# Optimization experiments

Measured on AMD Instinct MI355X. Metric: run time of the kernel, lower is better.

Reference implementation:

```python
import jax, jax.numpy as jnp
import numpy as np

D = 256; DFF = 1024; H = 8; L = 4; P = 4; NK = 18; NQ = 100; BS = 8; DH = D // H
SHAPES = ((100, 100), (50, 50), (25, 25), (13, 13))   # (H_l, W_l) per level
START = (0, 10000, 12500, 13125); LIN = 13294
PARAM_SHAPES = [
    ("across_in_w", (3 * D, D)), ("across_in_b", (3 * D,)), ("across_out_w", (D, D)), ("across_out_b", (D,)),
    ("within_in_w", (3 * D, D)), ("within_in_b", (3 * D,)), ("within_out_w", (D, D)), ("within_out_b", (D,)),
    ("off_w", (H * L * P * 2, D)), ("off_b", (H * L * P * 2,)), ("aw_w", (H * L * P, D)), ("aw_b", (H * L * P,)),
    ("val_w", (D, D)), ("val_b", (D,)), ("msout_w", (D, D)), ("msout_b", (D,)),
    ("lin1_w", (DFF, D)), ("lin1_b", (DFF,)), ("lin2_w", (D, DFF)), ("lin2_b", (D,)),
    ("lin1p_w", (DFF, D)), ("lin1p_b", (DFF,)), ("lin2p_w", (D, DFF)), ("lin2p_b", (D,)),
]
NORMS = ["across_norm", "within_norm", "norm1", "norm2", "norm2p"]
PNAMES = [n for n, _ in PARAM_SHAPES] + [n + s for n in NORMS for s in ("_g", "_b")]


def setup_inputs():
    ks = iter(jax.random.split(jax.random.key(0), 80))
    rn = lambda s, sc=1.0: jax.random.normal(next(ks), s, jnp.float32) * sc
    inp = {}
    inp["tgt_pose"] = rn((NQ, BS, NK, D))
    inp["tgt_pose_query_pos"] = rn((NQ, BS, NK, D))
    inp["tgt_pose_reference_points"] = jax.random.uniform(next(ks), (NQ * NK, BS, L, 2), jnp.float32)
    inp["memory"] = rn((LIN, BS, D))
    for n, s in PARAM_SHAPES:
        inp[n] = rn(s, 0.02)
    for n in NORMS:
        inp[n + "_g"] = 1.0 + rn((D,), 0.02)
        inp[n + "_b"] = rn((D,), 0.02)
    return inp


def _ln(x, g, b):
    mu = x.mean(-1, keepdims=True)
    xc = x - mu
    return xc * jax.lax.rsqrt((xc * xc).mean(-1, keepdims=True) + 1e-5) * g + b


def _mha(q, k, v, in_w, in_b, out_w, out_b, mask=None):
    # q,k,v: [S,B,D] (torch nn.MultiheadAttention layout)
    S, B, _ = q.shape
    def proj(x, i):
        return (x @ in_w[i * D:(i + 1) * D].T + in_b[i * D:(i + 1) * D]).reshape(-1, B, H, DH).transpose(1, 2, 0, 3)
    qh = proj(q, 0) * (DH ** -0.5); kh = proj(k, 1); vh = proj(v, 2)   # [B,H,S,DH]
    sc = jnp.einsum('bhqd,bhkd->bhqk', qh, kh)
    if mask is not None:
        sc = sc + mask
    o = jnp.einsum('bhqk,bhkd->bhqd', jax.nn.softmax(sc, -1), vh)
    return o.transpose(2, 0, 1, 3).reshape(S, B, D) @ out_w.T + out_b


def _msdeform(query, ref, mem, off_w, off_b, aw_w, aw_b, val_w, val_b, out_w, out_b):
    # query [N,Lq,D], ref [N,Lq,L,2] in [0,1] (x,y), mem [N,LIN,D]
    N, Lq, _ = query.shape
    value = (mem @ val_w.T + val_b).reshape(N, LIN, H, DH).transpose(0, 2, 1, 3)   # [N,H,LIN,DH]
    off = (query @ off_w.T + off_b).reshape(N, Lq, H, L, P, 2)
    aw = jax.nn.softmax((query @ aw_w.T + aw_b).reshape(N, Lq, H, L * P), -1).reshape(N, Lq, H, L, P)
    normalizer = jnp.array([[w, h] for (h, w) in SHAPES], jnp.float32)   # (W_l, H_l)
    loc = ref[:, :, None, :, None, :] + off / normalizer[None, None, None, :, None, :]   # [N,Lq,H,L,P,2]
    lvl_outs = []
    for li, (Hl, Wl) in enumerate(SHAPES):
        v_l = value[:, :, START[li]:START[li] + Hl * Wl]   # [N,H,Hl*Wl,DH]
        g = loc[:, :, :, li]                               # [N,Lq,H,P,2]
        # grid_sample(align_corners=False, padding_mode='zeros') on sampling grid 2*loc-1
        x = g[..., 0] * Wl - 0.5; y = g[..., 1] * Hl - 0.5
        x0 = jnp.floor(x); y0 = jnp.floor(y)
        lx = x - x0; ly = y - y0
        x0i = x0.astype(jnp.int32); y0i = y0.astype(jnp.int32)
        def gather(xi, yi):
            valid = ((xi >= 0) & (xi < Wl) & (yi >= 0) & (yi < Hl)).astype(v_l.dtype)
            idx = jnp.clip(yi, 0, Hl - 1) * Wl + jnp.clip(xi, 0, Wl - 1)   # [N,Lq,H,P]
            it = idx.transpose(0, 2, 1, 3).reshape(N, H, Lq * P)
            vt = jnp.take_along_axis(v_l, it[..., None], axis=2).reshape(N, H, Lq, P, DH)
            return vt * valid.transpose(0, 2, 1, 3)[..., None]
        wx = lx.transpose(0, 2, 1, 3)[..., None]; wy = ly.transpose(0, 2, 1, 3)[..., None]
        samp = (gather(x0i, y0i) * (1 - wx) * (1 - wy) + gather(x0i + 1, y0i) * wx * (1 - wy)
                + gather(x0i, y0i + 1) * (1 - wx) * wy + gather(x0i + 1, y0i + 1) * wx * wy)
        lvl_outs.append(samp)   # [N,H,Lq,P,DH]
    samp = jnp.stack(lvl_outs, 0)   # [L,N,H,Lq,P,DH]
    out = jnp.einsum('lnhqpd,nqhlp->nqhd', samp, aw).reshape(N, Lq, D)
    return out @ out_w.T + out_b


def _forward(tgt, pos, ref, mem, p):
    # 1) across-person self-attention along nq
    qf = tgt.reshape(NQ, BS * NK, D)
    t2 = _mha(qf, qf, qf, p['across_in_w'], p['across_in_b'], p['across_out_w'], p['across_out_b']).reshape(NQ, BS, NK, D)
    tgt = _ln(tgt + t2, p['across_norm_g'], p['across_norm_b'])
    # 2) deformable cross-attention; with_pos_embed mutates tgt in place in the original
    tgt = tgt + pos
    q = tgt.transpose(1, 0, 2, 3).reshape(BS, NQ * NK, D)
    t2 = _msdeform(q, ref.transpose(1, 0, 2, 3), mem.transpose(1, 0, 2),
                   p['off_w'], p['off_b'], p['aw_w'], p['aw_b'], p['val_w'], p['val_b'], p['msout_w'], p['msout_b'])
    t2 = t2.reshape(BS, NQ, NK, D).transpose(1, 0, 2, 3)
    tgt = _ln(tgt + t2, p['norm1_g'], p['norm1_b'])
    # 3) FFN
    t2 = jax.nn.relu(tgt @ p['lin1_w'].T + p['lin1_b']) @ p['lin2_w'].T + p['lin2_b']
    tgt = _ln(tgt + t2, p['norm2_g'], p['norm2_b'])
    # 4) within-pose self-attention (second in-place with_pos_embed)
    tgt = tgt + pos
    qw = tgt.reshape(NQ * BS, NK, D).transpose(1, 0, 2)
    mask = jnp.full((NK, NK), 1e-8, tgt.dtype)   # zero adjacency matrix additive mask
    t2 = _mha(qw, qw, qw, p['within_in_w'], p['within_in_b'], p['within_out_w'], p['within_out_b'], mask)
    t2 = t2.transpose(1, 0, 2).reshape(NQ, BS, NK, D)
    tgt = _ln(tgt + t2, p['within_norm_g'], p['within_norm_b'])
    # 5) late FFN
    t2 = jax.nn.relu(tgt @ p['lin1p_w'].T + p['lin1p_b']) @ p['lin2p_w'].T + p['lin2p_b']
    return _ln(tgt + t2, p['norm2p_g'], p['norm2p_b'])


def reference(tgt_pose, tgt_pose_query_pos, tgt_pose_reference_points, memory, across_in_w, across_in_b, across_out_w, across_out_b, within_in_w, within_in_b, within_out_w, within_out_b, off_w, off_b, aw_w, aw_b, val_w, val_b, msout_w, msout_b, lin1_w, lin1_b, lin2_w, lin2_b, lin1p_w, lin1p_b, lin2p_w, lin2p_b, across_norm_g, across_norm_b, within_norm_g, within_norm_b, norm1_g, norm1_b, norm2_g, norm2_b, norm2p_g, norm2p_b):
    _l = dict(locals())
    p = {n: _l[n] for n in PNAMES}
    return _forward(tgt_pose, tgt_pose_query_pos, tgt_pose_reference_points, memory, p)
```

## Files before the change

kernel.cpp:

```cpp
#include <hip/hip_runtime.h>
#include <cstdint>
#include <cstddef>

constexpr int D_   = 256;
constexpr int NK_  = 18;
constexpr int NQ_  = 100;
constexpr int BS_  = 8;
constexpr int T_   = NQ_ * BS_ * NK_;
constexpr int LIN_ = 13294;
constexpr int LQ_  = NQ_ * NK_;

typedef __attribute__((ext_vector_type(8))) short bfv8;
typedef __attribute__((ext_vector_type(4))) float f32x4;

__device__ __forceinline__ ushort f2b(float f) {
  uint32_t u = __builtin_bit_cast(uint32_t, f);
  u += 0x7fffu + ((u >> 16) & 1u);
  return (ushort)(u >> 16);
}
__device__ __forceinline__ float b2f(ushort h) {
  uint32_t u = ((uint32_t)h) << 16;
  return __builtin_bit_cast(float, u);
}
__device__ __forceinline__ uint pk2(float lo, float hi) {
  return (uint)f2b(lo) | ((uint)f2b(hi) << 16);
}
__device__ __forceinline__ void gload16(const ushort* g, ushort* l) {
  __builtin_amdgcn_global_load_lds(
      (const __attribute__((address_space(1))) void*)g,
      (__attribute__((address_space(3))) void*)l, 16, 0, 0);
}

constexpr int WOF0  = 0;
constexpr int WOF1  = 196608;
constexpr int WOF2  = 393216;
constexpr int WOF3  = 458752;
constexpr int WOF4  = 524288;
constexpr int WOF5  = 589824;
constexpr int WOF6  = 622592;
constexpr int WOF7  = 688128;
constexpr int WOF8  = 753664;
constexpr int WOF9  = 1015808;
constexpr int WOF10 = 1277952;
constexpr int WOF11 = 1540096;
constexpr int WTOT  = 1802240;

__global__ __launch_bounds__(256) void conv_weights(
    const float* __restrict__ w0, const float* __restrict__ w1,
    const float* __restrict__ w2, const float* __restrict__ w3,
    const float* __restrict__ w4, const float* __restrict__ w5,
    const float* __restrict__ w6, const float* __restrict__ w7,
    const float* __restrict__ w8, const float* __restrict__ w9,
    const float* __restrict__ w10, const float* __restrict__ w11,
    ushort* __restrict__ out) {
  int i8 = (blockIdx.x * 256 + threadIdx.x) * 8;
  if (i8 >= WTOT) return;
  const float* src; int off;
  if      (i8 < WOF1)  { src = w0;  off = WOF0; }
  else if (i8 < WOF2)  { src = w1;  off = WOF1; }
  else if (i8 < WOF3)  { src = w2;  off = WOF2; }
  else if (i8 < WOF4)  { src = w3;  off = WOF3; }
  else if (i8 < WOF5)  { src = w4;  off = WOF4; }
  else if (i8 < WOF6)  { src = w5;  off = WOF5; }
  else if (i8 < WOF7)  { src = w6;  off = WOF6; }
  else if (i8 < WOF8)  { src = w7;  off = WOF7; }
  else if (i8 < WOF9)  { src = w8;  off = WOF8; }
  else if (i8 < WOF10) { src = w9;  off = WOF9; }
  else if (i8 < WOF11) { src = w10; off = WOF10; }
  else                 { src = w11; off = WOF11; }
  const float4 v0 = *(const float4*)(src + (i8 - off));
  const float4 v1 = *(const float4*)(src + (i8 - off) + 4);
  uint4 o;
  o.x = pk2(v0.x, v0.y); o.y = pk2(v0.z, v0.w);
  o.z = pk2(v1.x, v1.y); o.w = pk2(v1.z, v1.w);
  *(uint4*)(out + i8) = o;
}

__global__ __launch_bounds__(384) void pack_bias(
    const float* __restrict__ off_b, const float* __restrict__ aw_b,
    float* __restrict__ out) {
  int t = threadIdx.x;
  out[t] = (t < 256) ? off_b[t] : aw_b[t - 256];
}

template<bool REORD>
__global__ __launch_bounds__(256) void conv_a_bf16(
    const float* __restrict__ in, ushort* __restrict__ out, int rows) {
  int idx = blockIdx.x * 256 + threadIdx.x;
  int r = idx >> 5, c = (idx & 31) * 8;
  if (r >= rows) return;
  int ro = r;
  if (REORD) { int i = r >> 3, b = r & 7; ro = b * LIN_ + i; }
  const float* p = in + (size_t)r * 256 + c;
  float4 v0 = *(const float4*)p, v1 = *(const float4*)(p + 4);
  uint4 o;
  o.x = pk2(v0.x, v0.y); o.y = pk2(v0.z, v0.w);
  o.z = pk2(v1.x, v1.y); o.w = pk2(v1.z, v1.w);
  *(uint4*)(out + (size_t)ro * 256 + c) = o;
}

template<int AMODE, int OUTMODE, int BM>
__global__ __launch_bounds__(256) void gemm_mfma(
    const ushort* __restrict__ A, const ushort* __restrict__ W,
    const float* __restrict__ bias, void* __restrict__ Cv,
    int M, int N, int K) {
  constexpr int AJ = BM / 64;
  constexpr int MR = BM / 32;
  __shared__ ushort As[BM * 32];
  __shared__ ushort Bs[128 * 32];
  const int tid = threadIdx.x;
  const int bm = blockIdx.y * BM, bn = blockIdx.x * 128;
  const int wave = tid >> 6, lane = tid & 63;

  const int srow = wave * 16 + (lane >> 2);
  const ushort* gA[AJ]; ushort* lA[AJ];
  const ushort* gB[2];  ushort* lB[2];
#pragma unroll
  for (int j = 0; j < AJ; ++j) {
    int row = j * 64 + srow;
    int gch = (lane & 3) ^ (row & 3);
    int gm = bm + row; if (gm >= M) gm = M - 1;
    int asrc;
    if (AMODE == 0) {
      asrc = gm;
    } else {
      int b = gm / LQ_, lq = gm - b * LQ_;
      int qq = lq / NK_, kk = lq - qq * NK_;
      asrc = qq * (BS_ * NK_) + b * NK_ + kk;
    }
    gA[j] = A + (size_t)asrc * K + gch * 8;
    lA[j] = As + (j * 4 + wave) * 512;
  }
#pragma unroll
  for (int j = 0; j < 2; ++j) {
    int row = j * 64 + srow;
    int gch = (lane & 3) ^ (row & 3);
    gB[j] = W + (size_t)(bn + row) * K + gch * 8;
    lB[j] = Bs + (j * 4 + wave) * 512;
  }

  const int wm = (wave >> 1) * (BM / 2), wn = (wave & 1) * 64;
  const int fr = lane & 15, fk = lane >> 4;
  const int sw = (fk ^ (fr & 3)) << 3;

  f32x4 acc[MR][4] = {};
  for (int k0 = 0; k0 < K; k0 += 32) {
#pragma unroll
    for (int j = 0; j < AJ; ++j) gload16(gA[j] + k0, lA[j]);
#pragma unroll
    for (int j = 0; j < 2; ++j) gload16(gB[j] + k0, lB[j]);
    __syncthreads();
    bfv8 a[MR], b[4];
#pragma unroll
    for (int m = 0; m < MR; ++m)
      a[m] = *(const bfv8*)&As[(wm + m * 16 + fr) * 32 + sw];
#pragma unroll
    for (int n = 0; n < 4; ++n)
      b[n] = *(const bfv8*)&Bs[(wn + n * 16 + fr) * 32 + sw];
#pragma unroll
    for (int m = 0; m < MR; ++m)
#pragma unroll
      for (int n = 0; n < 4; ++n)
        acc[m][n] = __builtin_amdgcn_mfma_f32_16x16x32_bf16(a[m], b[n], acc[m][n], 0, 0, 0);
    __syncthreads();
  }

  const int row0 = (lane >> 4) * 4;
  const int col = lane & 15;
#pragma unroll
  for (int m = 0; m < MR; ++m) {
#pragma unroll
    for (int n = 0; n < 4; ++n) {
      int cn = bn + wn + n * 16 + col;
      float bv = bias[cn];
#pragma unroll
      for (int j = 0; j < 4; ++j) {
        int mg = bm + wm + m * 16 + row0 + j;
        if (mg < M) {
          float o = acc[m][n][j] + bv;
          if (OUTMODE == 2) o = fmaxf(o, 0.f);
          if (OUTMODE == 0) ((float*)Cv)[(size_t)mg * N + cn] = o;
          else ((ushort*)Cv)[(size_t)mg * N + cn] = f2b(o);
        }
      }
    }
  }
}

template<int LNMODE>
__global__ __launch_bounds__(256) void gemm_ln(
    const ushort* __restrict__ A, const ushort* __restrict__ W,
    const float* __restrict__ bias, const float* __restrict__ X,
    const float* __restrict__ POS, const float* __restrict__ G,
    const float* __restrict__ Bb, float* __restrict__ CT,
    ushort* __restrict__ CTb, int K) {
  __shared__ float Ep[32][264];
  ushort* As = (ushort*)&Ep[0][0];
  ushort* Bs = As + 32 * 32;

  const int tid = threadIdx.x;
  const int wave = tid >> 6, lane = tid & 63;
  const int bm = blockIdx.x * 32;

  const int arow = wave * 8 + (lane >> 2);
  const int agch = (lane & 3) ^ (arow & 3);
  const ushort* gA = A + (size_t)(bm + arow) * K + agch * 8;
  ushort* lA = As + wave * 256;
  const int srow = wave * 16 + (lane >> 2);
  const ushort* gB[4]; ushort* lB[4];
#pragma unroll
  for (int j = 0; j < 4; ++j) {
    int row = j * 64 + srow;
    int gch = (lane & 3) ^ (row & 3);
    gB[j] = W + (size_t)row * K + gch * 8;
    lB[j] = Bs + (j * 4 + wave) * 512;
  }

  const int wn = wave * 64;
  const int fr = lane & 15, fk = lane >> 4;
  const int sw = (fk ^ (fr & 3)) << 3;

  f32x4 acc[2][4] = {};
  for (int k0 = 0; k0 < K; k0 += 32) {
    if (lane < 32) gload16(gA + k0, lA);
#pragma unroll
    for (int j = 0; j < 4; ++j) gload16(gB[j] + k0, lB[j]);
    __syncthreads();
    bfv8 a[2], b[4];
#pragma unroll
    for (int m = 0; m < 2; ++m)
      a[m] = *(const bfv8*)&As[(m * 16 + fr) * 32 + sw];
#pragma unroll
    for (int n = 0; n < 4; ++n)
      b[n] = *(const bfv8*)&Bs[(wn + n * 16 + fr) * 32 + sw];
#pragma unroll
    for (int m = 0; m < 2; ++m)
#pragma unroll
      for (int n = 0; n < 4; ++n)
        acc[m][n] = __builtin_amdgcn_mfma_f32_16x16x32_bf16(a[m], b[n], acc[m][n], 0, 0, 0);
    __syncthreads();
  }

  const int row0 = (lane >> 4) * 4;
  const int col = lane & 15;
  float bv[4];
#pragma unroll
  for (int n = 0; n < 4; ++n) bv[n] = bias[wn + n * 16 + col];

  const float4 g4 = *(const float4*)(G + lane * 4);
  const float4 bb4 = *(const float4*)(Bb + lane * 4);

#pragma unroll
  for (int m = 0; m < 2; ++m)
#pragma unroll
    for (int n = 0; n < 4; ++n)
#pragma unroll
      for (int j = 0; j < 4; ++j)
        Ep[m * 16 + row0 + j][wn + n * 16 + col] = acc[m][n][j] + bv[n];
  __syncthreads();

  for (int rr = 0; rr < 8; ++rr) {
    int lrow = wave * 8 + rr;
    size_t off = (size_t)(bm + lrow) * 256 + lane * 4;
    float4 ev = *(const float4*)&Ep[lrow][lane * 4];
    float4 xv = *(const float4*)(X + off);
    float4 v = make_float4(xv.x + ev.x, xv.y + ev.y, xv.z + ev.z, xv.w + ev.w);
    float s = v.x + v.y + v.z + v.w;
#pragma unroll
    for (int o = 32; o; o >>= 1) s += __shfl_xor(s, o);
    float mu = s * (1.0f / 256.0f);
    float4 c = make_float4(v.x - mu, v.y - mu, v.z - mu, v.w - mu);
    float q = c.x * c.x + c.y * c.y + c.z * c.z + c.w * c.w;
#pragma unroll
    for (int o = 32; o; o >>= 1) q += __shfl_xor(q, o);
    float rs = rsqrtf(q * (1.0f / 256.0f) + 1e-5f);
    float4 o4;
    o4.x = c.x * rs * g4.x + bb4.x;
    o4.y = c.y * rs * g4.y + bb4.y;
    o4.z = c.z * rs * g4.z + bb4.z;
    o4.w = c.w * rs * g4.w + bb4.w;
    if (LNMODE == 0) {
      float4 pv = *(const float4*)(POS + off);
      o4.x += pv.x; o4.y += pv.y; o4.z += pv.z; o4.w += pv.w;
    }
    *(float4*)(CT + off) = o4;
    if (LNMODE != 2) {
      ushort4 ob;
      ob.x = f2b(o4.x); ob.y = f2b(o4.y); ob.z = f2b(o4.z); ob.w = f2b(o4.w);
      *(ushort4*)(CTb + off) = ob;
    }
  }
}

__global__ __launch_bounds__(256) void attn_across_mfma(
    const ushort* __restrict__ QKV, ushort* __restrict__ O) {
  __shared__ ushort Qs[112][40];
  __shared__ ushort Ks[112][40];
  __shared__ ushort Vt[32][136];
  __shared__ ushort Ps[112][136];
  const int b = blockIdx.x >> 3, h = blockIdx.x & 7;
  const int tid = threadIdx.x;

  for (int idx = tid; idx < 112 * 16; idx += 256) {
    int r = idx >> 4, du = (idx & 15) * 2;
    uint q = 0, k = 0;
    if (r < 100) {
      size_t base = ((size_t)r * 144 + b) * 768 + h * 32 + du;
      q = *(const uint*)(QKV + base);
      k = *(const uint*)(QKV + base + 256);
    }
    *(uint*)&Qs[r][du] = q;
    *(uint*)&Ks[r][du] = k;
  }
  for (int idx = tid; idx < 128 * 32; idx += 256) {
    int s = idx >> 5, d = idx & 31;
    ushort v = 0;
    if (s < 100) v = QKV[((size_t)s * 144 + b) * 768 + 512 + h * 32 + d];
    Vt[d][s] = v;
  }
  for (int idx = tid; idx < 112 * 8; idx += 256) {
    int r = idx >> 3, c = 112 + (idx & 7) * 2;
    *(uint*)&Ps[r][c] = 0;
  }
  __syncthreads();

  const int wave = tid >> 6, lane = tid & 63;
  const int fr = lane & 15, fk = lane >> 4;
  const float scale = 0.17677669529663687f;

#pragma unroll
  for (int mi = 0; mi < 2; ++mi) {
    const int mt = wave + mi * 4;
    if (mt < 7) {
      bfv8 aq = *(const bfv8*)&Qs[mt * 16 + fr][fk * 8];
      f32x4 sacc[7];
#pragma unroll
      for (int nt = 0; nt < 7; ++nt) {
        bfv8 bk = *(const bfv8*)&Ks[nt * 16 + fr][fk * 8];
        f32x4 z = {0.f, 0.f, 0.f, 0.f};
        sacc[nt] = __builtin_amdgcn_mfma_f32_16x16x32_bf16(aq, bk, z, 0, 0, 0);
      }
      const bool maskc = (lane & 15) >= 4;
#pragma unroll
      for (int j = 0; j < 4; ++j) {
        float v[7];
        float mx = -1e30f;
#pragma unroll
        for (int nt = 0; nt < 7; ++nt) {
          float s = sacc[nt][j] * scale;
          if (nt == 6 && maskc) s = -1e30f;
          v[nt] = s;
          mx = fmaxf(mx, s);
        }
        mx = fmaxf(mx, __shfl_xor(mx, 1));
        mx = fmaxf(mx, __shfl_xor(mx, 2));
        mx = fmaxf(mx, __shfl_xor(mx, 4));
        mx = fmaxf(mx, __shfl_xor(mx, 8));
        float sum = 0.f;
#pragma unroll
        for (int nt = 0; nt < 7; ++nt) {
          v[nt] = __expf(v[nt] - mx);
          sum += v[nt];
        }
        sum += __shfl_xor(sum, 1);
        sum += __shfl_xor(sum, 2);
        sum += __shfl_xor(sum, 4);
        sum += __shfl_xor(sum, 8);
        float inv = 1.f / sum;
        int row = mt * 16 + (lane >> 4) * 4 + j;
#pragma unroll
        for (int nt = 0; nt < 7; ++nt)
          Ps[row][nt * 16 + (lane & 15)] = f2b(v[nt] * inv);
      }
    }
  }
  __syncthreads();

  f32x4 oacc[2][2] = {};
#pragma unroll
  for (int mi = 0; mi < 2; ++mi) {
    const int mt = wave + mi * 4;
    if (mt < 7) {
#pragma unroll
      for (int ks = 0; ks < 4; ++ks) {
        bfv8 ap = *(const bfv8*)&Ps[mt * 16 + fr][ks * 32 + fk * 8];
#pragma unroll
        for (int n = 0; n < 2; ++n) {
          bfv8 bv = *(const bfv8*)&Vt[n * 16 + fr][ks * 32 + fk * 8];
          oacc[mi][n] = __builtin_amdgcn_mfma_f32_16x16x32_bf16(ap, bv, oacc[mi][n], 0, 0, 0);
        }
      }
#pragma unroll
      for (int n = 0; n < 2; ++n) {
#pragma unroll
        for (int j = 0; j < 4; ++j) {
          int q = mt * 16 + (lane >> 4) * 4 + j;
          if (q < 100) {
            O[((size_t)q * 144 + b) * 256 + h * 32 + n * 16 + (lane & 15)] =
                f2b(oacc[mi][n][j]);
          }
        }
      }
    }
  }
}

__global__ __launch_bounds__(256) void attn_within(
    const ushort* __restrict__ QKV, ushort* __restrict__ O) {
  constexpr int ST = 258;
  __shared__ ushort Qs[18 * ST];
  __shared__ ushort Ks[18 * ST];
  __shared__ ushort Vs[18 * ST];
  const int bidx = blockIdx.x;
  const int qq = bidx >> 3, bb = bidx & 7;
  const int tid = threadIdx.x;
  for (int idx = tid; idx < 18 * 128; idx += 256) {
    int r = idx >> 7, j2 = (idx & 127) * 2;
    size_t base = ((size_t)qq * 144 + bb * 18 + r) * 768 + j2;
    *(uint*)&Qs[r * ST + j2] = *(const uint*)(QKV + base);
    *(uint*)&Ks[r * ST + j2] = *(const uint*)(QKV + base + 256);
    *(uint*)&Vs[r * ST + j2] = *(const uint*)(QKV + base + 512);
  }
  __syncthreads();
  const int wave = tid >> 6, lane = tid & 63;
  const int h = wave * 2 + (lane >> 5);
  const int li = lane & 31;
  const int hd = h * 32;
  const float scale = 0.17677669529663687f;
  const bool kv = li < 18;
  for (int s = 0; s < 18; ++s) {
    float sc = 0.f;
    if (kv) {
      const ushort* qrow = &Qs[s * ST + hd];
      const ushort* krow = &Ks[li * ST + hd];
#pragma unroll 8
      for (int d = 0; d < 32; ++d) sc += b2f(qrow[d]) * b2f(krow[d]);
    }
    sc = kv ? sc * scale : -1e30f;
    float mx = sc;
    mx = fmaxf(mx, __shfl_xor(mx, 16));
    mx = fmaxf(mx, __shfl_xor(mx, 8));
    mx = fmaxf(mx, __shfl_xor(mx, 4));
    mx = fmaxf(mx, __shfl_xor(mx, 2));
    mx = fmaxf(mx, __shfl_xor(mx, 1));
    float e = kv ? __expf(sc - mx) : 0.f;
    float sum = e;
    sum += __shfl_xor(sum, 16);
    sum += __shfl_xor(sum, 8);
    sum += __shfl_xor(sum, 4);
    sum += __shfl_xor(sum, 2);
    sum += __shfl_xor(sum, 1);
    float p = e / sum;
    float o = 0.f;
    const int half = lane & 32;
#pragma unroll
    for (int k = 0; k < 18; ++k) {
      float pk = __shfl(p, half + k);
      o += pk * b2f(Vs[k * ST + hd + li]);
    }
    O[((size_t)qq * 144 + bb * 18 + s) * 256 + hd + li] = f2b(o);
  }
}

__global__ __launch_bounds__(256) void deform_sample(
    const float* __restrict__ OFFAW, const ushort* __restrict__ V,
    const float* __restrict__ REF, ushort* __restrict__ OUT) {
  __shared__ uint2 sDesc[32 * 65];
  const int tid = threadIdx.x;
  const int m0 = blockIdx.x * 4;

  const int WH[4] = {100, 50, 25, 13};
  const int STl[4] = {0, 10000, 12500, 13125};

#pragma unroll
  for (int dd = 0; dd < 2; ++dd) {
    const int desc = tid + dd * 256;
    const int g = desc >> 7, rem = desc & 127;
    const int h = rem >> 4, lp = rem & 15, li = lp >> 2, p = lp & 3;
    const int m = m0 + g;
    const int b = m / LQ_, lq = m - b * LQ_;

    float awv = OFFAW[(size_t)m * 384 + 256 + h * 16 + lp];
    float mx = awv;
    mx = fmaxf(mx, __shfl_xor(mx, 8, 16));
    mx = fmaxf(mx, __shfl_xor(mx, 4, 16));
    mx = fmaxf(mx, __shfl_xor(mx, 2, 16));
    mx = fmaxf(mx, __shfl_xor(mx, 1, 16));
    float e = __expf(awv - mx);
    float sm = e;
    sm += __shfl_xor(sm, 8, 16);
    sm += __shfl_xor(sm, 4, 16);
    sm += __shfl_xor(sm, 2, 16);
    sm += __shfl_xor(sm, 1, 16);
    const float aw = e / sm;

    const float* offp = OFFAW + (size_t)m * 384 + h * 32 + li * 8 + p * 2;
    const float ox = offp[0], oy = offp[1];
    const float rx = REF[(((size_t)lq * 8 + b) * 4 + li) * 2 + 0];
    const float ry = REF[(((size_t)lq * 8 + b) * 4 + li) * 2 + 1];
    const int Wl = WH[li], st = STl[li];
    const float fW = (float)Wl;
    const float x = fmaf(rx, fW, ox) - 0.5f;
    const float y = fmaf(ry, fW, oy) - 0.5f;
    const float x0f = floorf(x), y0f = floorf(y);
    const float lx = x - x0f, ly = y - y0f;
    const int x0 = (int)x0f, y0 = (int)y0f;
    const int base = (g * 8 + h) * 65 + lp * 4;
#pragma unroll
    for (int c = 0; c < 4; ++c) {
      const int cx = c & 1, cy = c >> 1;
      const int xi = x0 + cx, yi = y0 + cy;
      const bool va = (xi >= 0) && (xi < Wl) && (yi >= 0) && (yi < Wl);
      const int xc = min(max(xi, 0), Wl - 1);
      const int yc = min(max(yi, 0), Wl - 1);
      const float wx = cx ? lx : (1.f - lx);
      const float wy = cy ? ly : (1.f - ly);
      const float wgt = va ? aw * wx * wy : 0.f;
      uint2 dv;
      dv.x = (uint)(st + yc * Wl + xc);
      dv.y = __builtin_bit_cast(uint, wgt);
      sDesc[base + c] = dv;
    }
  }
  __syncthreads();

  const int g = tid >> 6;
  const int h = (tid >> 3) & 7;
  const int d4 = (tid & 7) * 4;
  const int m = m0 + g;
  const int b = m / LQ_, lq = m - b * LQ_;
  const int qq = lq / NK_, kk = lq - qq * NK_;
  const ushort* Vg = V + ((size_t)b * LIN_) * 256 + h * 32 + d4;
  const int dbase = (g * 8 + h) * 65;
  float a0 = 0.f, a1 = 0.f, a2 = 0.f, a3 = 0.f;
#pragma unroll
  for (int lp = 0; lp < 16; ++lp) {
#pragma unroll
    for (int c = 0; c < 4; ++c) {
      const uint2 dv = sDesc[dbase + lp * 4 + c];
      const float w = __builtin_bit_cast(float, dv.y);
      const ushort4 v = *(const ushort4*)(Vg + (size_t)dv.x * 256);
      a0 = fmaf(w, b2f(v.x), a0);
      a1 = fmaf(w, b2f(v.y), a1);
      a2 = fmaf(w, b2f(v.z), a2);
      a3 = fmaf(w, b2f(v.w), a3);
    }
  }
  const size_t tok = (size_t)qq * 144 + b * 18 + kk;
  ushort4 o;
  o.x = f2b(a0); o.y = f2b(a1); o.z = f2b(a2); o.w = f2b(a3);
  *(ushort4*)(OUT + tok * 256 + h * 32 + d4) = o;
}

extern "C" void kernel_launch(void* const* d_in, const int* in_sizes, int n_in,
                              void* d_out, int out_size, void* d_ws, size_t ws_size,
                              hipStream_t stream) {
  const float* tgt  = (const float*)d_in[0];
  const float* pos  = (const float*)d_in[1];
  const float* ref  = (const float*)d_in[2];
  const float* mem  = (const float*)d_in[3];
  const float* across_in_w  = (const float*)d_in[4];
  const float* across_in_b  = (const float*)d_in[5];
  const float* across_out_w = (const float*)d_in[6];
  const float* across_out_b = (const float*)d_in[7];
  const float* within_in_w  = (const float*)d_in[8];
  const float* within_in_b  = (const float*)d_in[9];
  const float* within_out_w = (const float*)d_in[10];
  const float* within_out_b = (const float*)d_in[11];
  const float* off_w  = (const float*)d_in[12];
  const float* off_b  = (const float*)d_in[13];
  const float* aw_w   = (const float*)d_in[14];
  const float* aw_b   = (const float*)d_in[15];
  const float* val_w  = (const float*)d_in[16];
  const float* val_b  = (const float*)d_in[17];
  const float* msout_w = (const float*)d_in[18];
  const float* msout_b = (const float*)d_in[19];
  const float* lin1_w  = (const float*)d_in[20];
  const float* lin1_b  = (const float*)d_in[21];
  const float* lin2_w  = (const float*)d_in[22];
  const float* lin2_b  = (const float*)d_in[23];
  const float* lin1p_w = (const float*)d_in[24];
  const float* lin1p_b = (const float*)d_in[25];
  const float* lin2p_w = (const float*)d_in[26];
  const float* lin2p_b = (const float*)d_in[27];
  const float* across_norm_g = (const float*)d_in[28];
  const float* across_norm_b = (const float*)d_in[29];
  const float* within_norm_g = (const float*)d_in[30];
  const float* within_norm_b = (const float*)d_in[31];
  const float* norm1_g = (const float*)d_in[32];
  const float* norm1_b = (const float*)d_in[33];
  const float* norm2_g = (const float*)d_in[34];
  const float* norm2_b = (const float*)d_in[35];
  const float* norm2p_g = (const float*)d_in[36];
  const float* norm2p_b = (const float*)d_in[37];

  char* w = (char*)d_ws;
  ushort* Wb    = (ushort*)w;  w += 3604480;
  ushort* R1    = (ushort*)w;  w += (size_t)(BS_ * LIN_) * 256 * 2;
  ushort* AOb   = (ushort*)w;  w += (size_t)T_ * 256 * 2;
  float*  CT    = (float*)w;   w += (size_t)T_ * 256 * 4;
  ushort* CTb   = (ushort*)w;  w += (size_t)T_ * 256 * 2;
  ushort* Vb    = (ushort*)w;  w += (size_t)(BS_ * LIN_) * 256 * 2;
  float*  R2    = (float*)w;   w += (size_t)T_ * 384 * 4;
  float*  OAB   = (float*)w;   w += 384 * 4;
  ushort* memb  = R1;
  ushort* QKVb  = R1;
  ushort* tgtb  = (ushort*)R2;
  float*  OFFAW = R2;
  ushort* Uff   = Vb;
  ushort* SMPb  = AOb;

  ushort* W_across_in  = Wb + WOF0;
  ushort* W_within_in  = Wb + WOF1;
  ushort* W_across_out = Wb + WOF2;
  ushort* W_within_out = Wb + WOF3;
  ushort* W_offaw      = Wb + WOF4;
  ushort* W_val        = Wb + WOF6;
  ushort* W_msout      = Wb + WOF7;
  ushort* W_lin1       = Wb + WOF8;
  ushort* W_lin2       = Wb + WOF9;
  ushort* W_lin1p      = Wb + WOF10;
  ushort* W_lin2p      = Wb + WOF11;

  dim3 blk(256);
  const int MT = T_;
  const int MV = BS_ * LIN_;
  const int MVt = (MV + 127) / 128;
  const int MT64 = MT / 64;
  const int MT32 = MT / 32;

  conv_weights<<<dim3((WTOT / 8 + 255) / 256), blk, 0, stream>>>(
      across_in_w, within_in_w, across_out_w, within_out_w, off_w, aw_w,
      val_w, msout_w, lin1_w, lin2_w, lin1p_w, lin2p_w, Wb);
  pack_bias<<<dim3(1), dim3(384), 0, stream>>>(off_b, aw_b, OAB);
  conv_a_bf16<true><<<dim3(MV / 8), blk, 0, stream>>>(mem, memb, MV);
  conv_a_bf16<false><<<dim3(MT / 8), blk, 0, stream>>>(tgt, tgtb, MT);
  gemm_mfma<0, 1, 128><<<dim3(2, MVt), blk, 0, stream>>>(
      memb, W_val, val_b, Vb, MV, 256, 256);
  gemm_mfma<0, 1, 64><<<dim3(6, MT64), blk, 0, stream>>>(
      tgtb, W_across_in, across_in_b, QKVb, MT, 768, 256);
  attn_across_mfma<<<dim3(144 * 8), blk, 0, stream>>>(QKVb, AOb);
  gemm_ln<0><<<dim3(MT32), blk, 0, stream>>>(
      AOb, W_across_out, across_out_b, tgt, pos,
      across_norm_g, across_norm_b, CT, CTb, 256);
  gemm_mfma<2, 0, 64><<<dim3(3, MT64), blk, 0, stream>>>(
      CTb, W_offaw, OAB, OFFAW, MT, 384, 256);
  deform_sample<<<dim3(T_ / 4), blk, 0, stream>>>(OFFAW, Vb, ref, SMPb);
  gemm_ln<1><<<dim3(MT32), blk, 0, stream>>>(
      SMPb, W_msout, msout_b, CT, nullptr,
      norm1_g, norm1_b, CT, CTb, 256);
  gemm_mfma<0, 2, 64><<<dim3(8, MT64), blk, 0, stream>>>(
      CTb, W_lin1, lin1_b, Uff, MT, 1024, 256);
  gemm_ln<0><<<dim3(MT32), blk, 0, stream>>>(
      Uff, W_lin2, lin2_b, CT, pos,
      norm2_g, norm2_b, CT, CTb, 1024);
  gemm_mfma<0, 1, 64><<<dim3(6, MT64), blk, 0, stream>>>(
      CTb, W_within_in, within_in_b, QKVb, MT, 768, 256);
  attn_within<<<dim3(NQ_ * BS_), blk, 0, stream>>>(QKVb, AOb);
  gemm_ln<1><<<dim3(MT32), blk, 0, stream>>>(
      AOb, W_within_out, within_out_b, CT, nullptr,
      within_norm_g, within_norm_b, CT, CTb, 256);
  gemm_mfma<0, 2, 64><<<dim3(8, MT64), blk, 0, stream>>>(
      CTb, W_lin1p, lin1p_b, Uff, MT, 1024, 256);
  gemm_ln<2><<<dim3(MT32), blk, 0, stream>>>(
      Uff, W_lin2p, lin2p_b, CT, nullptr,
      norm2p_g, norm2p_b, (float*)d_out, nullptr, 1024);
}
```

Before: 401.1 us.

## Merge prologue conversion kernels and add full-width value-projection GEMM

```diff
diff --git a/kernel.cpp b/kernel.cpp
--- a/kernel.cpp
+++ b/kernel.cpp
@@ -52,7 +52,14 @@
     const float* __restrict__ w6, const float* __restrict__ w7,
     const float* __restrict__ w8, const float* __restrict__ w9,
     const float* __restrict__ w10, const float* __restrict__ w11,
-    ushort* __restrict__ out) {
+    ushort* __restrict__ out,
+    const float* __restrict__ off_b, const float* __restrict__ aw_b,
+    float* __restrict__ oab) {
+  if (blockIdx.x == 0) {
+    int t = threadIdx.x;
+    oab[t] = (t < 256) ? off_b[t] : aw_b[t - 256];
+    oab[t + 128] = (t + 128 < 256) ? off_b[t + 128] : aw_b[t - 128];
+  }
   int i8 = (blockIdx.x * 256 + threadIdx.x) * 8;
   if (i8 >= WTOT) return;
   const float* src; int off;
@@ -76,27 +83,29 @@
   *(uint4*)(out + i8) = o;
 }
 
-__global__ __launch_bounds__(384) void pack_bias(
-    const float* __restrict__ off_b, const float* __restrict__ aw_b,
-    float* __restrict__ out) {
-  int t = threadIdx.x;
-  out[t] = (t < 256) ? off_b[t] : aw_b[t - 256];
-}
-
-template<bool REORD>
-__global__ __launch_bounds__(256) void conv_a_bf16(
-    const float* __restrict__ in, ushort* __restrict__ out, int rows) {
+__global__ __launch_bounds__(256) void conv_acts(
+    const float* __restrict__ mem, ushort* __restrict__ memb,
+    const float* __restrict__ tgt, ushort* __restrict__ tgtb) {
   int idx = blockIdx.x * 256 + threadIdx.x;
   int r = idx >> 5, c = (idx & 31) * 8;
-  if (r >= rows) return;
-  int ro = r;
-  if (REORD) { int i = r >> 3, b = r & 7; ro = b * LIN_ + i; }
-  const float* p = in + (size_t)r * 256 + c;
+  const int MV = BS_ * LIN_;
+  const float* p;
+  ushort* q;
+  if (r < MV) {
+    int i = r >> 3, b = r & 7;
+    p = mem + (size_t)r * 256 + c;
+    q = memb + ((size_t)b * LIN_ + i) * 256 + c;
+  } else {
+    int rr = r - MV;
+    if (rr >= T_) return;
+    p = tgt + (size_t)rr * 256 + c;
+    q = tgtb + (size_t)rr * 256 + c;
+  }
   float4 v0 = *(const float4*)p, v1 = *(const float4*)(p + 4);
   uint4 o;
   o.x = pk2(v0.x, v0.y); o.y = pk2(v0.z, v0.w);
   o.z = pk2(v1.x, v1.y); o.w = pk2(v1.z, v1.w);
-  *(uint4*)(out + (size_t)ro * 256 + c) = o;
+  *(uint4*)q = o;
 }
 
 template<int AMODE, int OUTMODE, int BM>
@@ -182,6 +191,74 @@
           if (OUTMODE == 0) ((float*)Cv)[(size_t)mg * N + cn] = o;
           else ((ushort*)Cv)[(size_t)mg * N + cn] = f2b(o);
         }
+      }
+    }
+  }
+}
+
+__global__ __launch_bounds__(256) void gemm_wide(
+    const ushort* __restrict__ A, const ushort* __restrict__ W,
+    const float* __restrict__ bias, ushort* __restrict__ C,
+    int M, int K) {
+  __shared__ ushort As[32 * 32];
+  __shared__ ushort Bs[256 * 32];
+  const int tid = threadIdx.x;
+  const int wave = tid >> 6, lane = tid & 63;
+  const int bm = blockIdx.x * 32;
+
+  const int arow = wave * 8 + (lane >> 2);
+  int agm = bm + arow; if (agm >= M) agm = M - 1;
+  const int agch = (lane & 3) ^ (arow & 3);
+  const ushort* gA = A + (size_t)agm * K + agch * 8;
+  ushort* lA = As + wave * 256;
+  const int srow = wave * 16 + (lane >> 2);
+  const ushort* gB[4]; ushort* lB[4];
+#pragma unroll
+  for (int j = 0; j < 4; ++j) {
+    int row = j * 64 + srow;
+    int gch = (lane & 3) ^ (row & 3);
+    gB[j] = W + (size_t)row * K + gch * 8;
+    lB[j] = Bs + (j * 4 + wave) * 512;
+  }
+
+  const int wn = wave * 64;
+  const int fr = lane & 15, fk = lane >> 4;
+  const int sw = (fk ^ (fr & 3)) << 3;
+
+  f32x4 acc[2][4] = {};
+  for (int k0 = 0; k0 < K; k0 += 32) {
+    if (lane < 32) gload16(gA + k0, lA);
+#pragma unroll
+    for (int j = 0; j < 4; ++j) gload16(gB[j] + k0, lB[j]);
+    __syncthreads();
+    bfv8 a[2], b[4];
+#pragma unroll
+    for (int m = 0; m < 2; ++m)
+      a[m] = *(const bfv8*)&As[(m * 16 + fr) * 32 + sw];
+#pragma unroll
+    for (int n = 0; n < 4; ++n)
+      b[n] = *(const bfv8*)&Bs[(wn + n * 16 + fr) * 32 + sw];
+#pragma unroll
+    for (int m = 0; m < 2; ++m)
+#pragma unroll
+      for (int n = 0; n < 4; ++n)
+        acc[m][n] = __builtin_amdgcn_mfma_f32_16x16x32_bf16(a[m], b[n], acc[m][n], 0, 0, 0);
+    __syncthreads();
+  }
+
+  const int row0 = (lane >> 4) * 4;
+  const int col = lane & 15;
+#pragma unroll
+  for (int m = 0; m < 2; ++m) {
+#pragma unroll
+    for (int n = 0; n < 4; ++n) {
+      int cn = wn + n * 16 + col;
+      float bv = bias[cn];
+#pragma unroll
+      for (int j = 0; j < 4; ++j) {
+        int mg = bm + m * 16 + row0 + j;
+        if (mg < M)
+          C[(size_t)mg * 256 + cn] = f2b(acc[m][n][j] + bv);
       }
     }
   }
@@ -625,18 +702,17 @@
   dim3 blk(256);
   const int MT = T_;
   const int MV = BS_ * LIN_;
-  const int MVt = (MV + 127) / 128;
   const int MT64 = MT / 64;
   const int MT32 = MT / 32;
+  const int MV32 = (MV + 31) / 32;
 
   conv_weights<<<dim3((WTOT / 8 + 255) / 256), blk, 0, stream>>>(
       across_in_w, within_in_w, across_out_w, within_out_w, off_w, aw_w,
-      val_w, msout_w, lin1_w, lin2_w, lin1p_w, lin2p_w, Wb);
-  pack_bias<<<dim3(1), dim3(384), 0, stream>>>(off_b, aw_b, OAB);
-  conv_a_bf16<true><<<dim3(MV / 8), blk, 0, stream>>>(mem, memb, MV);
-  conv_a_bf16<false><<<dim3(MT / 8), blk, 0, stream>>>(tgt, tgtb, MT);
-  gemm_mfma<0, 1, 128><<<dim3(2, MVt), blk, 0, stream>>>(
-      memb, W_val, val_b, Vb, MV, 256, 256);
+      val_w, msout_w, lin1_w, lin2_w, lin1p_w, lin2p_w, Wb, off_b, aw_b, OAB);
+  conv_acts<<<dim3(((MV + MT) * 32 + 255) / 256), blk, 0, stream>>>(
+      mem, memb, tgt, tgtb);
+  gemm_wide<<<dim3(MV32), blk, 0, stream>>>(
+      memb, W_val, val_b, Vb, MV, 256);
   gemm_mfma<0, 1, 64><<<dim3(6, MT64), blk, 0, stream>>>(
       tgtb, W_across_in, across_in_b, QKVb, MT, 768, 256);
   attn_across_mfma<<<dim3(144 * 8), blk, 0, stream>>>(QKVb, AOb);
```

After: 403.2 us. Within noise of the previous version (+0.5%).
